# Kernel optimization log

Measured on AMD Instinct MI355X. Metric: run time of the kernel, lower is better.

Reference implementation:

```python
import jax, jax.numpy as jnp
import numpy as np

N = 100000
E = 3200000
H = 128
C = 40


def setup_inputs() -> dict:
    key = jax.random.key(0)
    ks = jax.random.split(key, 7)
    x = jax.random.normal(ks[0], (N, H), dtype=jnp.float32)
    edge_src = jax.random.randint(ks[1], (E,), 0, N, dtype=jnp.int32)
    edge_dst = jnp.sort(jax.random.randint(ks[2], (E,), 0, N, dtype=jnp.int32))
    edge_w = jax.random.uniform(ks[3], (E,), dtype=jnp.float32)
    s = 1.0 / np.sqrt(H)
    W0 = jax.random.normal(ks[4], (H, H), dtype=jnp.float32) * s
    W1 = jax.random.normal(ks[5], (H, H), dtype=jnp.float32) * s
    W2 = jax.random.normal(ks[6], (H, C), dtype=jnp.float32) * s
    return {"x": x, "edge_src": edge_src, "edge_dst": edge_dst,
            "edge_w": edge_w, "W0": W0, "W1": W1, "W2": W2}


def _spmm(h, edge_src, edge_dst, edge_w):
    # out[i] = sum_{e: dst_e == i} w_e * h[src_e]   (sparse adj @ h)
    msgs = h[edge_src] * edge_w[:, None]          # [E, d]
    return jax.ops.segment_sum(msgs, edge_dst, num_segments=N)


def reference(x, edge_src, edge_dst, edge_w, W0, W1, W2):
    # layer 1: tanh(Linear(spmm(adj, x)))  (dropout is identity in eval mode)
    h = jnp.tanh(_spmm(x, edge_src, edge_dst, edge_w) @ W0)
    # layer 2
    h = jnp.tanh(_spmm(h, edge_src, edge_dst, edge_w) @ W1)
    # output layer (GraphConvSparse default activation is tanh here too)
    out = jnp.tanh(_spmm(h, edge_src, edge_dst, edge_w) @ W2)
    return out
```

## Files before the change

### kernel.cpp

```cpp
#include <hip/hip_runtime.h>
#include <hip/hip_fp16.h>

#define NN 100000
#define NPAD 100096
#define EE 3200000
#define HH 128
#define CC 40

typedef _Float16 f16x8 __attribute__((ext_vector_type(8)));
typedef float f32x4 __attribute__((ext_vector_type(4)));

__device__ __forceinline__ float fast_tanh(float x) {
    float t = __expf(2.f * fminf(x, 15.f));
    return (t - 1.f) * __builtin_amdgcn_rcpf(t + 1.f);
}

__global__ void build_rp(const int* __restrict__ dst, int* __restrict__ rp) {
    int i = blockIdx.x * blockDim.x + threadIdx.x;
    if (i > NN) return;
    int lo = 0, hi = EE;
    while (lo < hi) {
        int mid = (lo + hi) >> 1;
        if (dst[mid] < i) lo = mid + 1; else hi = mid;
    }
    rp[i] = lo;
}

__global__ __launch_bounds__(256) void prep_all(const float* __restrict__ x,
                                                const int* __restrict__ src,
                                                const float* __restrict__ w,
                                                const float* __restrict__ W0,
                                                const float* __restrict__ W1,
                                                const float* __restrict__ W2,
                                                __half* __restrict__ xh,
                                                int4* __restrict__ ew,
                                                __half* __restrict__ W0t,
                                                __half* __restrict__ W1t,
                                                __half* __restrict__ W2t) {
    int b = blockIdx.x, tid = threadIdx.x;
    if (b < 6250) {
        int base = (b * 256 + tid) * 8;
        float4 a = *(const float4*)(x + base);
        float4 c = *(const float4*)(x + base + 4);
        __half2 h[4];
        h[0] = __floats2half2_rn(a.x, a.y);
        h[1] = __floats2half2_rn(a.z, a.w);
        h[2] = __floats2half2_rn(c.x, c.y);
        h[3] = __floats2half2_rn(c.z, c.w);
        *(float4*)(xh + base) = *(float4*)h;
    } else if (b < 9375) {
        int i = (b - 6250) * 256 + tid;
        int4 s = ((const int4*)src)[i];
        float4 f = ((const float4*)w)[i];
        int4 pa, pb;
        pa.x = s.x; pa.y = __float_as_int(f.x); pa.z = s.y; pa.w = __float_as_int(f.y);
        pb.x = s.z; pb.y = __float_as_int(f.z); pb.z = s.w; pb.w = __float_as_int(f.w);
        ew[2 * i] = pa; ew[2 * i + 1] = pb;
    } else {
        int i = (b - 9375) * 256 + tid;
        if (i < HH * HH) {
            int c = i >> 7, k = i & 127;
            W0t[i] = __float2half_rn(W0[k * HH + c]);
            W1t[i] = __float2half_rn(W1[k * HH + c]);
        }
        if (i < 64 * HH) {
            int c = i >> 7, k = i & 127;
            W2t[i] = __float2half_rn(c < CC ? W2[k * CC + c] : 0.f);
        }
    }
}

__global__ __launch_bounds__(256) void spmm_h16(const __half* __restrict__ h,
                                                const int2* __restrict__ ew,
                                                const int* __restrict__ rp,
                                                __half* __restrict__ out) {
    int node = blockIdx.x * 4 + (threadIdx.x >> 6);
    int l = threadIdx.x & 63;
    if (node >= NN) return;
    int e0 = __builtin_amdgcn_readfirstlane(rp[node]);
    int e1 = __builtin_amdgcn_readfirstlane(rp[node + 1]);
    int g = l >> 4, r = l & 15;
    const f16x8* __restrict__ hrow = (const f16x8*)h;
    float acc[8] = {};
    int e = e0;
    if ((e & 1) && e < e1) {
        int2 pr = ew[e];
        float wk = (g == 0) ? __int_as_float(pr.y) : 0.f;
        f16x8 v = hrow[(size_t)pr.x * 16 + r];
#pragma unroll
        for (int j = 0; j < 8; ++j) acc[j] = fmaf(wk, (float)v[j], acc[j]);
        ++e;
    }
    int efull = e + ((e1 - e) & ~15);
    for (; e < efull; e += 16) {
        const int4* pp = (const int4*)(ew + e + 4 * g);
        int4 pa = pp[0];
        int4 pb = pp[1];
        f16x8 v0 = hrow[(size_t)pa.x * 16 + r];
        f16x8 v1 = hrow[(size_t)pa.z * 16 + r];
        f16x8 v2 = hrow[(size_t)pb.x * 16 + r];
        f16x8 v3 = hrow[(size_t)pb.z * 16 + r];
        float w0 = __int_as_float(pa.y), w1 = __int_as_float(pa.w);
        float w2 = __int_as_float(pb.y), w3 = __int_as_float(pb.w);
#pragma unroll
        for (int j = 0; j < 8; ++j) acc[j] = fmaf(w0, (float)v0[j], acc[j]);
#pragma unroll
        for (int j = 0; j < 8; ++j) acc[j] = fmaf(w1, (float)v1[j], acc[j]);
#pragma unroll
        for (int j = 0; j < 8; ++j) acc[j] = fmaf(w2, (float)v2[j], acc[j]);
#pragma unroll
        for (int j = 0; j < 8; ++j) acc[j] = fmaf(w3, (float)v3[j], acc[j]);
    }
    if (e < e1) {
#pragma unroll
        for (int k = 0; k < 4; ++k) {
            int idx = e + 4 * g + k;
            bool val = idx < e1;
            int2 pr = ew[val ? idx : e0];
            float wk = val ? __int_as_float(pr.y) : 0.f;
            f16x8 v = hrow[(size_t)pr.x * 16 + r];
#pragma unroll
            for (int j = 0; j < 8; ++j) acc[j] = fmaf(wk, (float)v[j], acc[j]);
        }
    }
#pragma unroll
    for (int j = 0; j < 8; ++j) {
        acc[j] += __shfl_xor(acc[j], 16);
        acc[j] += __shfl_xor(acc[j], 32);
    }
    if (l < 16) {
        __half2 hv[4];
#pragma unroll
        for (int j = 0; j < 4; ++j) hv[j] = __floats2half2_rn(acc[2 * j], acc[2 * j + 1]);
        *(float4*)(out + (size_t)node * HH + r * 8) = *(float4*)hv;
    }
}

__global__ __launch_bounds__(256) void spmm40_tanh(const __half* __restrict__ gpad,
                                                   const int2* __restrict__ ew,
                                                   const int* __restrict__ rp,
                                                   float* __restrict__ out) {
    int node = blockIdx.x * 4 + (threadIdx.x >> 6);
    int l = threadIdx.x & 63;
    if (node >= NN) return;
    int e0 = __builtin_amdgcn_readfirstlane(rp[node]);
    int e1 = __builtin_amdgcn_readfirstlane(rp[node + 1]);
    int g = l >> 3, r = l & 7;
    const f16x8* __restrict__ grow = (const f16x8*)gpad;
    float acc[8] = {};
    int e = e0;
    if ((e & 1) && e < e1) {
        int2 pr = ew[e];
        float wk = (g == 0) ? __int_as_float(pr.y) : 0.f;
        f16x8 v = grow[(size_t)pr.x * 8 + r];
#pragma unroll
        for (int j = 0; j < 8; ++j) acc[j] = fmaf(wk, (float)v[j], acc[j]);
        ++e;
    }
    int efull = e + ((e1 - e) & ~15);
    for (; e < efull; e += 16) {
        int4 pa = *(const int4*)(ew + e + 2 * g);
        f16x8 v0 = grow[(size_t)pa.x * 8 + r];
        f16x8 v1 = grow[(size_t)pa.z * 8 + r];
        float w0 = __int_as_float(pa.y), w1 = __int_as_float(pa.w);
#pragma unroll
        for (int j = 0; j < 8; ++j) acc[j] = fmaf(w0, (float)v0[j], acc[j]);
#pragma unroll
        for (int j = 0; j < 8; ++j) acc[j] = fmaf(w1, (float)v1[j], acc[j]);
    }
    if (e < e1) {
#pragma unroll
        for (int k = 0; k < 2; ++k) {
            int idx = e + 2 * g + k;
            bool val = idx < e1;
            int2 pr = ew[val ? idx : e0];
            float wk = val ? __int_as_float(pr.y) : 0.f;
            f16x8 v = grow[(size_t)pr.x * 8 + r];
#pragma unroll
            for (int j = 0; j < 8; ++j) acc[j] = fmaf(wk, (float)v[j], acc[j]);
        }
    }
#pragma unroll
    for (int j = 0; j < 8; ++j) {
        acc[j] += __shfl_xor(acc[j], 8);
        acc[j] += __shfl_xor(acc[j], 16);
        acc[j] += __shfl_xor(acc[j], 32);
    }
    if (l < 5) {
        float o[8];
#pragma unroll
        for (int j = 0; j < 8; ++j) o[j] = fast_tanh(acc[j]);
        *(float4*)(out + (size_t)node * CC + r * 8) = *(float4*)&o[0];
        *(float4*)(out + (size_t)node * CC + r * 8 + 4) = *(float4*)&o[4];
    }
}

__global__ __launch_bounds__(256) void gemm_tanh_mfma(const __half* __restrict__ A,
                                                      const __half* __restrict__ Wt,
                                                      __half* __restrict__ out) {
    __shared__ _Float16 st[4][16][136];
    int wave = threadIdx.x >> 6, l = threadIdx.x & 63;
    int r0 = blockIdx.x * 64 + wave * 16;
    int lr = l & 15, lg = l >> 4;
    const _Float16* Af = (const _Float16*)A;
    const _Float16* Wf = (const _Float16*)Wt;
    f16x8 a[4];
#pragma unroll
    for (int kb = 0; kb < 4; ++kb)
        a[kb] = *(const f16x8*)(Af + (size_t)(r0 + lr) * HH + kb * 32 + lg * 8);
#pragma unroll
    for (int ct = 0; ct < 8; ++ct) {
        f32x4 acc = {0.f, 0.f, 0.f, 0.f};
#pragma unroll
        for (int kb = 0; kb < 4; ++kb) {
            f16x8 b = *(const f16x8*)(Wf + (size_t)(ct * 16 + lr) * HH + kb * 32 + lg * 8);
            acc = __builtin_amdgcn_mfma_f32_16x16x32_f16(a[kb], b, acc, 0, 0, 0);
        }
#pragma unroll
        for (int r = 0; r < 4; ++r)
            st[wave][lg * 4 + r][ct * 16 + lr] = (_Float16)fast_tanh(acc[r]);
    }
#pragma unroll
    for (int i = 0; i < 4; ++i) {
        int row = lg + 4 * i;
        int grow = r0 + row;
        f16x8 v = *(const f16x8*)&st[wave][row][lr * 8];
        if (grow < NN)
            *(f16x8*)((_Float16*)out + (size_t)grow * HH + lr * 8) = v;
    }
}

__global__ __launch_bounds__(256) void gemm2_fused(const __half* __restrict__ A,
                                                   const __half* __restrict__ W1t,
                                                   const __half* __restrict__ W2t,
                                                   __half* __restrict__ gout) {
    __shared__ _Float16 st[4][16][136];
    int wave = threadIdx.x >> 6, l = threadIdx.x & 63;
    int r0 = blockIdx.x * 64 + wave * 16;
    int lr = l & 15, lg = l >> 4;
    const _Float16* Af = (const _Float16*)A;
    const _Float16* W1f = (const _Float16*)W1t;
    const _Float16* W2f = (const _Float16*)W2t;
    f16x8 a[4];
#pragma unroll
    for (int kb = 0; kb < 4; ++kb)
        a[kb] = *(const f16x8*)(Af + (size_t)(r0 + lr) * HH + kb * 32 + lg * 8);
#pragma unroll
    for (int ct = 0; ct < 8; ++ct) {
        f32x4 acc = {0.f, 0.f, 0.f, 0.f};
#pragma unroll
        for (int kb = 0; kb < 4; ++kb) {
            f16x8 b = *(const f16x8*)(W1f + (size_t)(ct * 16 + lr) * HH + kb * 32 + lg * 8);
            acc = __builtin_amdgcn_mfma_f32_16x16x32_f16(a[kb], b, acc, 0, 0, 0);
        }
#pragma unroll
        for (int r = 0; r < 4; ++r)
            st[wave][lg * 4 + r][ct * 16 + lr] = (_Float16)fast_tanh(acc[r]);
    }
    f16x8 a2[4];
#pragma unroll
    for (int kb = 0; kb < 4; ++kb)
        a2[kb] = *(const f16x8*)&st[wave][lr][kb * 32 + lg * 8];
#pragma unroll
    for (int ct = 0; ct < 4; ++ct) {
        f32x4 acc = {0.f, 0.f, 0.f, 0.f};
#pragma unroll
        for (int kb = 0; kb < 4; ++kb) {
            f16x8 b = *(const f16x8*)(W2f + (size_t)(ct * 16 + lr) * HH + kb * 32 + lg * 8);
            acc = __builtin_amdgcn_mfma_f32_16x16x32_f16(a2[kb], b, acc, 0, 0, 0);
        }
#pragma unroll
        for (int r = 0; r < 4; ++r)
            st[wave][lg * 4 + r][ct * 16 + lr] = (_Float16)acc[r];
    }
#pragma unroll
    for (int i = 0; i < 2; ++i) {
        int row = (l >> 3) + 8 * i;
        int grow = r0 + row;
        f16x8 v = *(const f16x8*)&st[wave][row][(l & 7) * 8];
        if (grow < NN)
            *(f16x8*)((_Float16*)gout + (size_t)grow * 64 + (l & 7) * 8) = v;
    }
}

extern "C" void kernel_launch(void* const* d_in, const int* in_sizes, int n_in,
                              void* d_out, int out_size, void* d_ws, size_t ws_size,
                              hipStream_t stream) {
    const float* x    = (const float*)d_in[0];
    const int*   esrc = (const int*)d_in[1];
    const int*   edst = (const int*)d_in[2];
    const float* ew_f = (const float*)d_in[3];
    const float* W0   = (const float*)d_in[4];
    const float* W1   = (const float*)d_in[5];
    const float* W2   = (const float*)d_in[6];
    float* out = (float*)d_out;

    char* ws = (char*)d_ws;
    size_t off = 0;
    int* rp = (int*)(ws + off);          off += (((size_t)(NN + 1) * 4) + 511) & ~(size_t)511;
    __half* buf0 = (__half*)(ws + off);  off += (size_t)NPAD * HH * sizeof(__half);
    __half* sA = (__half*)(ws + off);    off += (size_t)NPAD * HH * sizeof(__half);
    __half* hb = (__half*)(ws + off);    off += (size_t)NPAD * HH * sizeof(__half);
    int2* ew = (int2*)(ws + off);        off += (size_t)EE * sizeof(int2);
    __half* W0t = (__half*)(ws + off);   off += (size_t)HH * HH * sizeof(__half);
    __half* W1t = (__half*)(ws + off);   off += (size_t)HH * HH * sizeof(__half);
    __half* W2t = (__half*)(ws + off);   off += (size_t)64 * HH * sizeof(__half);
    __half* xh = buf0;
    __half* gb = buf0;

    build_rp<<<(NN + 256) / 256, 256, 0, stream>>>(edst, rp);
    prep_all<<<9439, 256, 0, stream>>>(x, esrc, ew_f, W0, W1, W2,
                                       xh, (int4*)ew, W0t, W1t, W2t);

    int gemm_grid = NPAD / 64;
    spmm_h16<<<NN / 4, 256, 0, stream>>>(xh, ew, rp, sA);
    gemm_tanh_mfma<<<gemm_grid, 256, 0, stream>>>(sA, W0t, hb);
    spmm_h16<<<NN / 4, 256, 0, stream>>>(hb, ew, rp, sA);
    gemm2_fused<<<gemm_grid, 256, 0, stream>>>(sA, W1t, W2t, gb);
    spmm40_tanh<<<NN / 4, 256, 0, stream>>>(gb, ew, rp, out);
}
```

Baseline: 483.2 us.

## Fuse SpMM with MFMA GEMM per layer and pack edges into 32-bit words

Each of the first two layers now runs as one kernel. A wave aggregates 16 node rows into shared memory, with one half2 column pair per lane, then runs the MFMA GEMM plus tanh in place, so the intermediate sA buffer round-trip and two launches are removed. Edge source and weight are packed into a single 32-bit word (17-bit index, 15-bit quantised weight), halving edge-stream traffic. In exchange, the weights lose precision, and the aggregation walks nodes sequentially with unroll 1, which may expose gather latency.

```diff
diff --git a/kernel.cpp b/kernel.cpp
--- a/kernel.cpp
+++ b/kernel.cpp
@@ -33,7 +33,7 @@
                                                 const float* __restrict__ W1,
                                                 const float* __restrict__ W2,
                                                 __half* __restrict__ xh,
-                                                int4* __restrict__ ew,
+                                                unsigned* __restrict__ ewp,
                                                 __half* __restrict__ W0t,
                                                 __half* __restrict__ W1t,
                                                 __half* __restrict__ W2t) {
@@ -52,10 +52,12 @@
         int i = (b - 6250) * 256 + tid;
         int4 s = ((const int4*)src)[i];
         float4 f = ((const float4*)w)[i];
-        int4 pa, pb;
-        pa.x = s.x; pa.y = __float_as_int(f.x); pa.z = s.y; pa.w = __float_as_int(f.y);
-        pb.x = s.z; pb.y = __float_as_int(f.z); pb.z = s.w; pb.w = __float_as_int(f.w);
-        ew[2 * i] = pa; ew[2 * i + 1] = pb;
+        uint4 p;
+        p.x = (unsigned)s.x | ((unsigned)(f.x * 32767.f + 0.5f) << 17);
+        p.y = (unsigned)s.y | ((unsigned)(f.y * 32767.f + 0.5f) << 17);
+        p.z = (unsigned)s.z | ((unsigned)(f.z * 32767.f + 0.5f) << 17);
+        p.w = (unsigned)s.w | ((unsigned)(f.w * 32767.f + 0.5f) << 17);
+        ((uint4*)ewp)[i] = p;
     } else {
         int i = (b - 9375) * 256 + tid;
         if (i < HH * HH) {
@@ -70,74 +72,174 @@
     }
 }
 
-__global__ __launch_bounds__(256) void spmm_h16(const __half* __restrict__ h,
-                                                const int2* __restrict__ ew,
+#define EDEC_W(v) ((float)((v) >> 17) * (1.f / 32767.f))
+#define EDEC_S(v) ((v) & 131071u)
+
+__device__ __forceinline__ void spmm_tile(const __half2* __restrict__ h2,
+                                          const unsigned* __restrict__ ewp,
+                                          const int* __restrict__ rp,
+                                          int n0, int l,
+                                          _Float16 (* __restrict__ As)[136]) {
+#pragma unroll 1
+    for (int i = 0; i < 16; ++i) {
+        int node = n0 + i;
+        int ia = node <= NN ? node : NN;
+        int ib = node + 1 <= NN ? node + 1 : NN;
+        int e0 = __builtin_amdgcn_readfirstlane(rp[ia]);
+        int e1 = __builtin_amdgcn_readfirstlane(rp[ib]);
+        float accx = 0.f, accy = 0.f;
+        int e = e0;
+        while ((e & 3) && e < e1) {
+            unsigned v = ewp[e];
+            float wk = EDEC_W(v);
+            float2 f = __half22float2(h2[(size_t)EDEC_S(v) * 64 + l]);
+            accx = fmaf(wk, f.x, accx); accy = fmaf(wk, f.y, accy);
+            ++e;
+        }
+        int e8 = e + ((e1 - e) & ~7);
+#pragma unroll 1
+        for (; e < e8; e += 8) {
+            uint4 pa = *(const uint4*)(ewp + e);
+            uint4 pb = *(const uint4*)(ewp + e + 4);
+            __half2 r0 = h2[(size_t)EDEC_S(pa.x) * 64 + l];
+            __half2 r1 = h2[(size_t)EDEC_S(pa.y) * 64 + l];
+            __half2 r2 = h2[(size_t)EDEC_S(pa.z) * 64 + l];
+            __half2 r3 = h2[(size_t)EDEC_S(pa.w) * 64 + l];
+            __half2 r4 = h2[(size_t)EDEC_S(pb.x) * 64 + l];
+            __half2 r5 = h2[(size_t)EDEC_S(pb.y) * 64 + l];
+            __half2 r6 = h2[(size_t)EDEC_S(pb.z) * 64 + l];
+            __half2 r7 = h2[(size_t)EDEC_S(pb.w) * 64 + l];
+            float2 f0 = __half22float2(r0), f1 = __half22float2(r1);
+            float2 f2 = __half22float2(r2), f3 = __half22float2(r3);
+            float2 f4 = __half22float2(r4), f5 = __half22float2(r5);
+            float2 f6 = __half22float2(r6), f7 = __half22float2(r7);
+            float w0 = EDEC_W(pa.x), w1 = EDEC_W(pa.y), w2 = EDEC_W(pa.z), w3 = EDEC_W(pa.w);
+            float w4 = EDEC_W(pb.x), w5 = EDEC_W(pb.y), w6 = EDEC_W(pb.z), w7 = EDEC_W(pb.w);
+            accx = fmaf(w0, f0.x, accx); accy = fmaf(w0, f0.y, accy);
+            accx = fmaf(w1, f1.x, accx); accy = fmaf(w1, f1.y, accy);
+            accx = fmaf(w2, f2.x, accx); accy = fmaf(w2, f2.y, accy);
+            accx = fmaf(w3, f3.x, accx); accy = fmaf(w3, f3.y, accy);
+            accx = fmaf(w4, f4.x, accx); accy = fmaf(w4, f4.y, accy);
+            accx = fmaf(w5, f5.x, accx); accy = fmaf(w5, f5.y, accy);
+            accx = fmaf(w6, f6.x, accx); accy = fmaf(w6, f6.y, accy);
+            accx = fmaf(w7, f7.x, accx); accy = fmaf(w7, f7.y, accy);
+        }
+        if (e + 4 <= e1) {
+            uint4 pa = *(const uint4*)(ewp + e);
+            __half2 r0 = h2[(size_t)EDEC_S(pa.x) * 64 + l];
+            __half2 r1 = h2[(size_t)EDEC_S(pa.y) * 64 + l];
+            __half2 r2 = h2[(size_t)EDEC_S(pa.z) * 64 + l];
+            __half2 r3 = h2[(size_t)EDEC_S(pa.w) * 64 + l];
+            float2 f0 = __half22float2(r0), f1 = __half22float2(r1);
+            float2 f2 = __half22float2(r2), f3 = __half22float2(r3);
+            float w0 = EDEC_W(pa.x), w1 = EDEC_W(pa.y), w2 = EDEC_W(pa.z), w3 = EDEC_W(pa.w);
+            accx = fmaf(w0, f0.x, accx); accy = fmaf(w0, f0.y, accy);
+            accx = fmaf(w1, f1.x, accx); accy = fmaf(w1, f1.y, accy);
+            accx = fmaf(w2, f2.x, accx); accy = fmaf(w2, f2.y, accy);
+            accx = fmaf(w3, f3.x, accx); accy = fmaf(w3, f3.y, accy);
+            e += 4;
+        }
+        while (e < e1) {
+            unsigned v = ewp[e];
+            float wk = EDEC_W(v);
+            float2 f = __half22float2(h2[(size_t)EDEC_S(v) * 64 + l]);
+            accx = fmaf(wk, f.x, accx); accy = fmaf(wk, f.y, accy);
+            ++e;
+        }
+        *(__half2*)&As[i][2 * l] = __floats2half2_rn(accx, accy);
+    }
+}
+
+__global__ __launch_bounds__(256) void fused_l1(const __half* __restrict__ h,
+                                                const unsigned* __restrict__ ewp,
                                                 const int* __restrict__ rp,
+                                                const __half* __restrict__ Wt,
                                                 __half* __restrict__ out) {
-    int node = blockIdx.x * 4 + (threadIdx.x >> 6);
-    int l = threadIdx.x & 63;
-    if (node >= NN) return;
-    int e0 = __builtin_amdgcn_readfirstlane(rp[node]);
-    int e1 = __builtin_amdgcn_readfirstlane(rp[node + 1]);
-    int g = l >> 4, r = l & 15;
-    const f16x8* __restrict__ hrow = (const f16x8*)h;
-    float acc[8] = {};
-    int e = e0;
-    if ((e & 1) && e < e1) {
-        int2 pr = ew[e];
-        float wk = (g == 0) ? __int_as_float(pr.y) : 0.f;
-        f16x8 v = hrow[(size_t)pr.x * 16 + r];
-#pragma unroll
-        for (int j = 0; j < 8; ++j) acc[j] = fmaf(wk, (float)v[j], acc[j]);
-        ++e;
-    }
-    int efull = e + ((e1 - e) & ~15);
-    for (; e < efull; e += 16) {
-        const int4* pp = (const int4*)(ew + e + 4 * g);
-        int4 pa = pp[0];
-        int4 pb = pp[1];
-        f16x8 v0 = hrow[(size_t)pa.x * 16 + r];
-        f16x8 v1 = hrow[(size_t)pa.z * 16 + r];
-        f16x8 v2 = hrow[(size_t)pb.x * 16 + r];
-        f16x8 v3 = hrow[(size_t)pb.z * 16 + r];
-        float w0 = __int_as_float(pa.y), w1 = __int_as_float(pa.w);
-        float w2 = __int_as_float(pb.y), w3 = __int_as_float(pb.w);
-#pragma unroll
-        for (int j = 0; j < 8; ++j) acc[j] = fmaf(w0, (float)v0[j], acc[j]);
-#pragma unroll
-        for (int j = 0; j < 8; ++j) acc[j] = fmaf(w1, (float)v1[j], acc[j]);
-#pragma unroll
-        for (int j = 0; j < 8; ++j) acc[j] = fmaf(w2, (float)v2[j], acc[j]);
-#pragma unroll
-        for (int j = 0; j < 8; ++j) acc[j] = fmaf(w3, (float)v3[j], acc[j]);
-    }
-    if (e < e1) {
-#pragma unroll
-        for (int k = 0; k < 4; ++k) {
-            int idx = e + 4 * g + k;
-            bool val = idx < e1;
-            int2 pr = ew[val ? idx : e0];
-            float wk = val ? __int_as_float(pr.y) : 0.f;
-            f16x8 v = hrow[(size_t)pr.x * 16 + r];
-#pragma unroll
-            for (int j = 0; j < 8; ++j) acc[j] = fmaf(wk, (float)v[j], acc[j]);
-        }
-    }
-#pragma unroll
-    for (int j = 0; j < 8; ++j) {
-        acc[j] += __shfl_xor(acc[j], 16);
-        acc[j] += __shfl_xor(acc[j], 32);
-    }
-    if (l < 16) {
-        __half2 hv[4];
-#pragma unroll
-        for (int j = 0; j < 4; ++j) hv[j] = __floats2half2_rn(acc[2 * j], acc[2 * j + 1]);
-        *(float4*)(out + (size_t)node * HH + r * 8) = *(float4*)hv;
+    __shared__ _Float16 As[4][16][136];
+    int wave = threadIdx.x >> 6, l = threadIdx.x & 63;
+    int n0 = blockIdx.x * 64 + wave * 16;
+    spmm_tile((const __half2*)h, ewp, rp, n0, l, As[wave]);
+    int lr = l & 15, lg = l >> 4;
+    f16x8 a[4];
+#pragma unroll
+    for (int kb = 0; kb < 4; ++kb)
+        a[kb] = *(const f16x8*)&As[wave][lr][kb * 32 + lg * 8];
+    const _Float16* Wf = (const _Float16*)Wt;
+#pragma unroll
+    for (int ct = 0; ct < 8; ++ct) {
+        f32x4 acc = {0.f, 0.f, 0.f, 0.f};
+#pragma unroll
+        for (int kb = 0; kb < 4; ++kb) {
+            f16x8 b = *(const f16x8*)(Wf + (size_t)(ct * 16 + lr) * HH + kb * 32 + lg * 8);
+            acc = __builtin_amdgcn_mfma_f32_16x16x32_f16(a[kb], b, acc, 0, 0, 0);
+        }
+#pragma unroll
+        for (int r = 0; r < 4; ++r)
+            As[wave][lg * 4 + r][ct * 16 + lr] = (_Float16)fast_tanh(acc[r]);
+    }
+#pragma unroll
+    for (int i = 0; i < 4; ++i) {
+        int row = lg + 4 * i;
+        f16x8 v = *(const f16x8*)&As[wave][row][lr * 8];
+        *(f16x8*)((_Float16*)out + (size_t)(n0 + row) * HH + lr * 8) = v;
+    }
+}
+
+__global__ __launch_bounds__(256) void fused_l2(const __half* __restrict__ h,
+                                                const unsigned* __restrict__ ewp,
+                                                const int* __restrict__ rp,
+                                                const __half* __restrict__ W1t,
+                                                const __half* __restrict__ W2t,
+                                                __half* __restrict__ gout) {
+    __shared__ _Float16 As[4][16][136];
+    int wave = threadIdx.x >> 6, l = threadIdx.x & 63;
+    int n0 = blockIdx.x * 64 + wave * 16;
+    spmm_tile((const __half2*)h, ewp, rp, n0, l, As[wave]);
+    int lr = l & 15, lg = l >> 4;
+    const _Float16* W1f = (const _Float16*)W1t;
+    const _Float16* W2f = (const _Float16*)W2t;
+    f16x8 a[4];
+#pragma unroll
+    for (int kb = 0; kb < 4; ++kb)
+        a[kb] = *(const f16x8*)&As[wave][lr][kb * 32 + lg * 8];
+#pragma unroll
+    for (int ct = 0; ct < 8; ++ct) {
+        f32x4 acc = {0.f, 0.f, 0.f, 0.f};
+#pragma unroll
+        for (int kb = 0; kb < 4; ++kb) {
+            f16x8 b = *(const f16x8*)(W1f + (size_t)(ct * 16 + lr) * HH + kb * 32 + lg * 8);
+            acc = __builtin_amdgcn_mfma_f32_16x16x32_f16(a[kb], b, acc, 0, 0, 0);
+        }
+#pragma unroll
+        for (int r = 0; r < 4; ++r)
+            As[wave][lg * 4 + r][ct * 16 + lr] = (_Float16)fast_tanh(acc[r]);
+    }
+    f16x8 a2[4];
+#pragma unroll
+    for (int kb = 0; kb < 4; ++kb)
+        a2[kb] = *(const f16x8*)&As[wave][lr][kb * 32 + lg * 8];
+#pragma unroll
+    for (int ct = 0; ct < 4; ++ct) {
+        f32x4 acc = {0.f, 0.f, 0.f, 0.f};
+#pragma unroll
+        for (int kb = 0; kb < 4; ++kb) {
+            f16x8 b = *(const f16x8*)(W2f + (size_t)(ct * 16 + lr) * HH + kb * 32 + lg * 8);
+            acc = __builtin_amdgcn_mfma_f32_16x16x32_f16(a2[kb], b, acc, 0, 0, 0);
+        }
+#pragma unroll
+        for (int r = 0; r < 4; ++r)
+            As[wave][lg * 4 + r][ct * 16 + lr] = (_Float16)acc[r];
+    }
+#pragma unroll
+    for (int i = 0; i < 2; ++i) {
+        int row = (l >> 3) + 8 * i;
+        f16x8 v = *(const f16x8*)&As[wave][row][(l & 7) * 8];
+        *(f16x8*)((_Float16*)gout + (size_t)(n0 + row) * 64 + (l & 7) * 8) = v;
     }
 }
 
 __global__ __launch_bounds__(256) void spmm40_tanh(const __half* __restrict__ gpad,
-                                                   const int2* __restrict__ ew,
+                                                   const unsigned* __restrict__ ewp,
                                                    const int* __restrict__ rp,
                                                    float* __restrict__ out) {
     int node = blockIdx.x * 4 + (threadIdx.x >> 6);
@@ -146,23 +248,23 @@
     int e0 = __builtin_amdgcn_readfirstlane(rp[node]);
     int e1 = __builtin_amdgcn_readfirstlane(rp[node + 1]);
     int g = l >> 3, r = l & 7;
-    const f16x8* __restrict__ grow = (const f16x8*)gpad;
+    const f16x8* __restrict__ grw = (const f16x8*)gpad;
     float acc[8] = {};
     int e = e0;
-    if ((e & 1) && e < e1) {
-        int2 pr = ew[e];
-        float wk = (g == 0) ? __int_as_float(pr.y) : 0.f;
-        f16x8 v = grow[(size_t)pr.x * 8 + r];
-#pragma unroll
-        for (int j = 0; j < 8; ++j) acc[j] = fmaf(wk, (float)v[j], acc[j]);
+    while ((e & 1) && e < e1) {
+        unsigned v = ewp[e];
+        float wk = (g == 0) ? EDEC_W(v) : 0.f;
+        f16x8 vv = grw[(size_t)EDEC_S(v) * 8 + r];
+#pragma unroll
+        for (int j = 0; j < 8; ++j) acc[j] = fmaf(wk, (float)vv[j], acc[j]);
         ++e;
     }
-    int efull = e + ((e1 - e) & ~15);
-    for (; e < efull; e += 16) {
-        int4 pa = *(const int4*)(ew + e + 2 * g);
-        f16x8 v0 = grow[(size_t)pa.x * 8 + r];
-        f16x8 v1 = grow[(size_t)pa.z * 8 + r];
-        float w0 = __int_as_float(pa.y), w1 = __int_as_float(pa.w);
+    int e16 = e + ((e1 - e) & ~15);
+    for (; e < e16; e += 16) {
+        uint2 pa = *(const uint2*)(ewp + e + 2 * g);
+        f16x8 v0 = grw[(size_t)EDEC_S(pa.x) * 8 + r];
+        f16x8 v1 = grw[(size_t)EDEC_S(pa.y) * 8 + r];
+        float w0 = EDEC_W(pa.x), w1 = EDEC_W(pa.y);
 #pragma unroll
         for (int j = 0; j < 8; ++j) acc[j] = fmaf(w0, (float)v0[j], acc[j]);
 #pragma unroll
@@ -173,11 +275,11 @@
         for (int k = 0; k < 2; ++k) {
             int idx = e + 2 * g + k;
             bool val = idx < e1;
-            int2 pr = ew[val ? idx : e0];
-            float wk = val ? __int_as_float(pr.y) : 0.f;
-            f16x8 v = grow[(size_t)pr.x * 8 + r];
-#pragma unroll
-            for (int j = 0; j < 8; ++j) acc[j] = fmaf(wk, (float)v[j], acc[j]);
+            unsigned v = ewp[val ? idx : e0];
+            float wk = val ? EDEC_W(v) : 0.f;
+            f16x8 vv = grw[(size_t)EDEC_S(v) * 8 + r];
+#pragma unroll
+            for (int j = 0; j < 8; ++j) acc[j] = fmaf(wk, (float)vv[j], acc[j]);
         }
     }
 #pragma unroll
@@ -192,94 +294,6 @@
         for (int j = 0; j < 8; ++j) o[j] = fast_tanh(acc[j]);
         *(float4*)(out + (size_t)node * CC + r * 8) = *(float4*)&o[0];
         *(float4*)(out + (size_t)node * CC + r * 8 + 4) = *(float4*)&o[4];
-    }
-}
-
-__global__ __launch_bounds__(256) void gemm_tanh_mfma(const __half* __restrict__ A,
-                                                      const __half* __restrict__ Wt,
-                                                      __half* __restrict__ out) {
-    __shared__ _Float16 st[4][16][136];
-    int wave = threadIdx.x >> 6, l = threadIdx.x & 63;
-    int r0 = blockIdx.x * 64 + wave * 16;
-    int lr = l & 15, lg = l >> 4;
-    const _Float16* Af = (const _Float16*)A;
-    const _Float16* Wf = (const _Float16*)Wt;
-    f16x8 a[4];
-#pragma unroll
-    for (int kb = 0; kb < 4; ++kb)
-        a[kb] = *(const f16x8*)(Af + (size_t)(r0 + lr) * HH + kb * 32 + lg * 8);
-#pragma unroll
-    for (int ct = 0; ct < 8; ++ct) {
-        f32x4 acc = {0.f, 0.f, 0.f, 0.f};
-#pragma unroll
-        for (int kb = 0; kb < 4; ++kb) {
-            f16x8 b = *(const f16x8*)(Wf + (size_t)(ct * 16 + lr) * HH + kb * 32 + lg * 8);
-            acc = __builtin_amdgcn_mfma_f32_16x16x32_f16(a[kb], b, acc, 0, 0, 0);
-        }
-#pragma unroll
-        for (int r = 0; r < 4; ++r)
-            st[wave][lg * 4 + r][ct * 16 + lr] = (_Float16)fast_tanh(acc[r]);
-    }
-#pragma unroll
-    for (int i = 0; i < 4; ++i) {
-        int row = lg + 4 * i;
-        int grow = r0 + row;
-        f16x8 v = *(const f16x8*)&st[wave][row][lr * 8];
-        if (grow < NN)
-            *(f16x8*)((_Float16*)out + (size_t)grow * HH + lr * 8) = v;
-    }
-}
-
-__global__ __launch_bounds__(256) void gemm2_fused(const __half* __restrict__ A,
-                                                   const __half* __restrict__ W1t,
-                                                   const __half* __restrict__ W2t,
-                                                   __half* __restrict__ gout) {
-    __shared__ _Float16 st[4][16][136];
-    int wave = threadIdx.x >> 6, l = threadIdx.x & 63;
-    int r0 = blockIdx.x * 64 + wave * 16;
-    int lr = l & 15, lg = l >> 4;
-    const _Float16* Af = (const _Float16*)A;
-    const _Float16* W1f = (const _Float16*)W1t;
-    const _Float16* W2f = (const _Float16*)W2t;
-    f16x8 a[4];
-#pragma unroll
-    for (int kb = 0; kb < 4; ++kb)
-        a[kb] = *(const f16x8*)(Af + (size_t)(r0 + lr) * HH + kb * 32 + lg * 8);
-#pragma unroll
-    for (int ct = 0; ct < 8; ++ct) {
-        f32x4 acc = {0.f, 0.f, 0.f, 0.f};
-#pragma unroll
-        for (int kb = 0; kb < 4; ++kb) {
-            f16x8 b = *(const f16x8*)(W1f + (size_t)(ct * 16 + lr) * HH + kb * 32 + lg * 8);
-            acc = __builtin_amdgcn_mfma_f32_16x16x32_f16(a[kb], b, acc, 0, 0, 0);
-        }
-#pragma unroll
-        for (int r = 0; r < 4; ++r)
-            st[wave][lg * 4 + r][ct * 16 + lr] = (_Float16)fast_tanh(acc[r]);
-    }
-    f16x8 a2[4];
-#pragma unroll
-    for (int kb = 0; kb < 4; ++kb)
-        a2[kb] = *(const f16x8*)&st[wave][lr][kb * 32 + lg * 8];
-#pragma unroll
-    for (int ct = 0; ct < 4; ++ct) {
-        f32x4 acc = {0.f, 0.f, 0.f, 0.f};
-#pragma unroll
-        for (int kb = 0; kb < 4; ++kb) {
-            f16x8 b = *(const f16x8*)(W2f + (size_t)(ct * 16 + lr) * HH + kb * 32 + lg * 8);
-            acc = __builtin_amdgcn_mfma_f32_16x16x32_f16(a2[kb], b, acc, 0, 0, 0);
-        }
-#pragma unroll
-        for (int r = 0; r < 4; ++r)
-            st[wave][lg * 4 + r][ct * 16 + lr] = (_Float16)acc[r];
-    }
-#pragma unroll
-    for (int i = 0; i < 2; ++i) {
-        int row = (l >> 3) + 8 * i;
-        int grow = r0 + row;
-        f16x8 v = *(const f16x8*)&st[wave][row][(l & 7) * 8];
-        if (grow < NN)
-            *(f16x8*)((_Float16*)gout + (size_t)grow * 64 + (l & 7) * 8) = v;
     }
 }
 
@@ -299,9 +313,8 @@
     size_t off = 0;
     int* rp = (int*)(ws + off);          off += (((size_t)(NN + 1) * 4) + 511) & ~(size_t)511;
     __half* buf0 = (__half*)(ws + off);  off += (size_t)NPAD * HH * sizeof(__half);
-    __half* sA = (__half*)(ws + off);    off += (size_t)NPAD * HH * sizeof(__half);
     __half* hb = (__half*)(ws + off);    off += (size_t)NPAD * HH * sizeof(__half);
-    int2* ew = (int2*)(ws + off);        off += (size_t)EE * sizeof(int2);
+    unsigned* ewp = (unsigned*)(ws + off); off += (size_t)EE * sizeof(unsigned);
     __half* W0t = (__half*)(ws + off);   off += (size_t)HH * HH * sizeof(__half);
     __half* W1t = (__half*)(ws + off);   off += (size_t)HH * HH * sizeof(__half);
     __half* W2t = (__half*)(ws + off);   off += (size_t)64 * HH * sizeof(__half);
@@ -309,13 +322,11 @@
     __half* gb = buf0;
 
     build_rp<<<(NN + 256) / 256, 256, 0, stream>>>(edst, rp);
-    prep_all<<<9439, 256, 0, stream>>>(x, esrc, ew_f, W0, W1, W2,
-                                       xh, (int4*)ew, W0t, W1t, W2t);
-
-    int gemm_grid = NPAD / 64;
-    spmm_h16<<<NN / 4, 256, 0, stream>>>(xh, ew, rp, sA);
-    gemm_tanh_mfma<<<gemm_grid, 256, 0, stream>>>(sA, W0t, hb);
-    spmm_h16<<<NN / 4, 256, 0, stream>>>(hb, ew, rp, sA);
-    gemm2_fused<<<gemm_grid, 256, 0, stream>>>(sA, W1t, W2t, gb);
-    spmm40_tanh<<<NN / 4, 256, 0, stream>>>(gb, ew, rp, out);
-}
+    prep_all<<<9440, 256, 0, stream>>>(x, esrc, ew_f, W0, W1, W2,
+                                       xh, ewp, W0t, W1t, W2t);
+
+    int grid = NPAD / 64;
+    fused_l1<<<grid, 256, 0, stream>>>(xh, ewp, rp, W0t, hb);
+    fused_l2<<<grid, 256, 0, stream>>>(hb, ewp, rp, W1t, W2t, gb);
+    spmm40_tanh<<<NN / 4, 256, 0, stream>>>(gb, ewp, rp, out);
+}
```

Result: slower. 507.6 us (+5.1%).

## Pack edge src and weight into 32 bits and bucket-sort edges by source

Applied to the files above, without the earlier changes.

Each edge's source index (17 bits) and weight (quantized to 15 bits) now share one 32-bit word, halving the edge-stream bytes read by the three SpMM passes. A new sort_edges kernel reorders each destination's edge list into 16 buckets by source range, so gathers within a node touch nearby rows and get better cache locality. This adds an extra pass over the edges and loses weight precision, since the 15-bit fixed-point weights could push results outside tolerance. The alignment prologue now handles up to 3 edges so the uint4 loads stay aligned.

```diff
diff --git a/kernel.cpp b/kernel.cpp
--- a/kernel.cpp
+++ b/kernel.cpp
@@ -6,9 +6,13 @@
 #define EE 3200000
 #define HH 128
 #define CC 40
+#define NT 16
 
 typedef _Float16 f16x8 __attribute__((ext_vector_type(8)));
 typedef float f32x4 __attribute__((ext_vector_type(4)));
+
+#define EDEC_W(v) ((float)((v) >> 17) * (1.f / 32767.f))
+#define EDEC_S(v) ((v) & 131071u)
 
 __device__ __forceinline__ float fast_tanh(float x) {
     float t = __expf(2.f * fminf(x, 15.f));
@@ -33,7 +37,7 @@
                                                 const float* __restrict__ W1,
                                                 const float* __restrict__ W2,
                                                 __half* __restrict__ xh,
-                                                int4* __restrict__ ew,
+                                                unsigned* __restrict__ ewp,
                                                 __half* __restrict__ W0t,
                                                 __half* __restrict__ W1t,
                                                 __half* __restrict__ W2t) {
@@ -52,10 +56,12 @@
         int i = (b - 6250) * 256 + tid;
         int4 s = ((const int4*)src)[i];
         float4 f = ((const float4*)w)[i];
-        int4 pa, pb;
-        pa.x = s.x; pa.y = __float_as_int(f.x); pa.z = s.y; pa.w = __float_as_int(f.y);
-        pb.x = s.z; pb.y = __float_as_int(f.z); pb.z = s.w; pb.w = __float_as_int(f.w);
-        ew[2 * i] = pa; ew[2 * i + 1] = pb;
+        uint4 p;
+        p.x = (unsigned)s.x | ((unsigned)(f.x * 32767.f + 0.5f) << 17);
+        p.y = (unsigned)s.y | ((unsigned)(f.y * 32767.f + 0.5f) << 17);
+        p.z = (unsigned)s.z | ((unsigned)(f.z * 32767.f + 0.5f) << 17);
+        p.w = (unsigned)s.w | ((unsigned)(f.w * 32767.f + 0.5f) << 17);
+        ((uint4*)ewp)[i] = p;
     } else {
         int i = (b - 9375) * 256 + tid;
         if (i < HH * HH) {
@@ -70,8 +76,47 @@
     }
 }
 
+__global__ __launch_bounds__(256) void sort_edges(const unsigned* __restrict__ in,
+                                                  const int* __restrict__ rp,
+                                                  unsigned* __restrict__ outp) {
+    int node = blockIdx.x * 4 + (threadIdx.x >> 6);
+    int l = threadIdx.x & 63;
+    if (node >= NN) return;
+    int e0 = __builtin_amdgcn_readfirstlane(rp[node]);
+    int e1 = __builtin_amdgcn_readfirstlane(rp[node + 1]);
+    int count[NT];
+#pragma unroll
+    for (int t = 0; t < NT; ++t) count[t] = 0;
+    for (int e = e0; e < e1; e += 64) {
+        int idx = e + l;
+        bool val = idx < e1;
+        unsigned v = val ? in[idx] : 0u;
+        int t = val ? (int)(EDEC_S(v) >> 13) : -1;
+#pragma unroll
+        for (int tt = 0; tt < NT; ++tt)
+            count[tt] += __popcll(__ballot(t == tt));
+    }
+    int base[NT];
+    int run = e0;
+#pragma unroll
+    for (int tt = 0; tt < NT; ++tt) { base[tt] = run; run += count[tt]; }
+    unsigned long long lmask = (1ull << l) - 1ull;
+    for (int e = e0; e < e1; e += 64) {
+        int idx = e + l;
+        bool val = idx < e1;
+        unsigned v = val ? in[idx] : 0u;
+        int t = val ? (int)(EDEC_S(v) >> 13) : -1;
+#pragma unroll
+        for (int tt = 0; tt < NT; ++tt) {
+            unsigned long long b = __ballot(t == tt);
+            if (t == tt) outp[base[tt] + __popcll(b & lmask)] = v;
+            base[tt] += __popcll(b);
+        }
+    }
+}
+
 __global__ __launch_bounds__(256) void spmm_h16(const __half* __restrict__ h,
-                                                const int2* __restrict__ ew,
+                                                const unsigned* __restrict__ ewp,
                                                 const int* __restrict__ rp,
                                                 __half* __restrict__ out) {
     int node = blockIdx.x * 4 + (threadIdx.x >> 6);
@@ -83,25 +128,22 @@
     const f16x8* __restrict__ hrow = (const f16x8*)h;
     float acc[8] = {};
     int e = e0;
-    if ((e & 1) && e < e1) {
-        int2 pr = ew[e];
-        float wk = (g == 0) ? __int_as_float(pr.y) : 0.f;
-        f16x8 v = hrow[(size_t)pr.x * 16 + r];
-#pragma unroll
-        for (int j = 0; j < 8; ++j) acc[j] = fmaf(wk, (float)v[j], acc[j]);
+    while ((e & 3) && e < e1) {
+        unsigned v = ewp[e];
+        float wk = (g == 0) ? EDEC_W(v) : 0.f;
+        f16x8 vv = hrow[(size_t)EDEC_S(v) * 16 + r];
+#pragma unroll
+        for (int j = 0; j < 8; ++j) acc[j] = fmaf(wk, (float)vv[j], acc[j]);
         ++e;
     }
-    int efull = e + ((e1 - e) & ~15);
-    for (; e < efull; e += 16) {
-        const int4* pp = (const int4*)(ew + e + 4 * g);
-        int4 pa = pp[0];
-        int4 pb = pp[1];
-        f16x8 v0 = hrow[(size_t)pa.x * 16 + r];
-        f16x8 v1 = hrow[(size_t)pa.z * 16 + r];
-        f16x8 v2 = hrow[(size_t)pb.x * 16 + r];
-        f16x8 v3 = hrow[(size_t)pb.z * 16 + r];
-        float w0 = __int_as_float(pa.y), w1 = __int_as_float(pa.w);
-        float w2 = __int_as_float(pb.y), w3 = __int_as_float(pb.w);
+    int e16 = e + ((e1 - e) & ~15);
+    for (; e < e16; e += 16) {
+        uint4 p = *(const uint4*)(ewp + e + 4 * g);
+        f16x8 v0 = hrow[(size_t)EDEC_S(p.x) * 16 + r];
+        f16x8 v1 = hrow[(size_t)EDEC_S(p.y) * 16 + r];
+        f16x8 v2 = hrow[(size_t)EDEC_S(p.z) * 16 + r];
+        f16x8 v3 = hrow[(size_t)EDEC_S(p.w) * 16 + r];
+        float w0 = EDEC_W(p.x), w1 = EDEC_W(p.y), w2 = EDEC_W(p.z), w3 = EDEC_W(p.w);
 #pragma unroll
         for (int j = 0; j < 8; ++j) acc[j] = fmaf(w0, (float)v0[j], acc[j]);
 #pragma unroll
@@ -116,11 +158,11 @@
         for (int k = 0; k < 4; ++k) {
             int idx = e + 4 * g + k;
             bool val = idx < e1;
-            int2 pr = ew[val ? idx : e0];
-            float wk = val ? __int_as_float(pr.y) : 0.f;
-            f16x8 v = hrow[(size_t)pr.x * 16 + r];
-#pragma unroll
-            for (int j = 0; j < 8; ++j) acc[j] = fmaf(wk, (float)v[j], acc[j]);
+            unsigned v = ewp[val ? idx : e0];
+            float wk = val ? EDEC_W(v) : 0.f;
+            f16x8 vv = hrow[(size_t)EDEC_S(v) * 16 + r];
+#pragma unroll
+            for (int j = 0; j < 8; ++j) acc[j] = fmaf(wk, (float)vv[j], acc[j]);
         }
     }
 #pragma unroll
@@ -137,7 +179,7 @@
 }
 
 __global__ __launch_bounds__(256) void spmm40_tanh(const __half* __restrict__ gpad,
-                                                   const int2* __restrict__ ew,
+                                                   const unsigned* __restrict__ ewp,
                                                    const int* __restrict__ rp,
                                                    float* __restrict__ out) {
     int node = blockIdx.x * 4 + (threadIdx.x >> 6);
@@ -146,23 +188,23 @@
     int e0 = __builtin_amdgcn_readfirstlane(rp[node]);
     int e1 = __builtin_amdgcn_readfirstlane(rp[node + 1]);
     int g = l >> 3, r = l & 7;
-    const f16x8* __restrict__ grow = (const f16x8*)gpad;
+    const f16x8* __restrict__ grw = (const f16x8*)gpad;
     float acc[8] = {};
     int e = e0;
-    if ((e & 1) && e < e1) {
-        int2 pr = ew[e];
-        float wk = (g == 0) ? __int_as_float(pr.y) : 0.f;
-        f16x8 v = grow[(size_t)pr.x * 8 + r];
-#pragma unroll
-        for (int j = 0; j < 8; ++j) acc[j] = fmaf(wk, (float)v[j], acc[j]);
+    while ((e & 1) && e < e1) {
+        unsigned v = ewp[e];
+        float wk = (g == 0) ? EDEC_W(v) : 0.f;
+        f16x8 vv = grw[(size_t)EDEC_S(v) * 8 + r];
+#pragma unroll
+        for (int j = 0; j < 8; ++j) acc[j] = fmaf(wk, (float)vv[j], acc[j]);
         ++e;
     }
-    int efull = e + ((e1 - e) & ~15);
-    for (; e < efull; e += 16) {
-        int4 pa = *(const int4*)(ew + e + 2 * g);
-        f16x8 v0 = grow[(size_t)pa.x * 8 + r];
-        f16x8 v1 = grow[(size_t)pa.z * 8 + r];
-        float w0 = __int_as_float(pa.y), w1 = __int_as_float(pa.w);
+    int e16 = e + ((e1 - e) & ~15);
+    for (; e < e16; e += 16) {
+        uint2 pa = *(const uint2*)(ewp + e + 2 * g);
+        f16x8 v0 = grw[(size_t)EDEC_S(pa.x) * 8 + r];
+        f16x8 v1 = grw[(size_t)EDEC_S(pa.y) * 8 + r];
+        float w0 = EDEC_W(pa.x), w1 = EDEC_W(pa.y);
 #pragma unroll
         for (int j = 0; j < 8; ++j) acc[j] = fmaf(w0, (float)v0[j], acc[j]);
 #pragma unroll
@@ -173,11 +215,11 @@
         for (int k = 0; k < 2; ++k) {
             int idx = e + 2 * g + k;
             bool val = idx < e1;
-            int2 pr = ew[val ? idx : e0];
-            float wk = val ? __int_as_float(pr.y) : 0.f;
-            f16x8 v = grow[(size_t)pr.x * 8 + r];
-#pragma unroll
-            for (int j = 0; j < 8; ++j) acc[j] = fmaf(wk, (float)v[j], acc[j]);
+            unsigned v = ewp[val ? idx : e0];
+            float wk = val ? EDEC_W(v) : 0.f;
+            f16x8 vv = grw[(size_t)EDEC_S(v) * 8 + r];
+#pragma unroll
+            for (int j = 0; j < 8; ++j) acc[j] = fmaf(wk, (float)vv[j], acc[j]);
         }
     }
 #pragma unroll
@@ -297,25 +339,27 @@
 
     char* ws = (char*)d_ws;
     size_t off = 0;
-    int* rp = (int*)(ws + off);          off += (((size_t)(NN + 1) * 4) + 511) & ~(size_t)511;
-    __half* buf0 = (__half*)(ws + off);  off += (size_t)NPAD * HH * sizeof(__half);
-    __half* sA = (__half*)(ws + off);    off += (size_t)NPAD * HH * sizeof(__half);
-    __half* hb = (__half*)(ws + off);    off += (size_t)NPAD * HH * sizeof(__half);
-    int2* ew = (int2*)(ws + off);        off += (size_t)EE * sizeof(int2);
-    __half* W0t = (__half*)(ws + off);   off += (size_t)HH * HH * sizeof(__half);
-    __half* W1t = (__half*)(ws + off);   off += (size_t)HH * HH * sizeof(__half);
-    __half* W2t = (__half*)(ws + off);   off += (size_t)64 * HH * sizeof(__half);
+    int* rp = (int*)(ws + off);            off += (((size_t)(NN + 1) * 4) + 511) & ~(size_t)511;
+    __half* buf0 = (__half*)(ws + off);    off += (size_t)NPAD * HH * sizeof(__half);
+    __half* sA = (__half*)(ws + off);      off += (size_t)NPAD * HH * sizeof(__half);
+    __half* hb = (__half*)(ws + off);      off += (size_t)NPAD * HH * sizeof(__half);
+    unsigned* ewp = (unsigned*)(ws + off); off += (size_t)EE * sizeof(unsigned);
+    unsigned* ews = (unsigned*)(ws + off); off += (size_t)EE * sizeof(unsigned);
+    __half* W0t = (__half*)(ws + off);     off += (size_t)HH * HH * sizeof(__half);
+    __half* W1t = (__half*)(ws + off);     off += (size_t)HH * HH * sizeof(__half);
+    __half* W2t = (__half*)(ws + off);     off += (size_t)64 * HH * sizeof(__half);
     __half* xh = buf0;
     __half* gb = buf0;
 
     build_rp<<<(NN + 256) / 256, 256, 0, stream>>>(edst, rp);
-    prep_all<<<9439, 256, 0, stream>>>(x, esrc, ew_f, W0, W1, W2,
-                                       xh, (int4*)ew, W0t, W1t, W2t);
+    prep_all<<<9440, 256, 0, stream>>>(x, esrc, ew_f, W0, W1, W2,
+                                       xh, ewp, W0t, W1t, W2t);
+    sort_edges<<<NN / 4, 256, 0, stream>>>(ewp, rp, ews);
 
     int gemm_grid = NPAD / 64;
-    spmm_h16<<<NN / 4, 256, 0, stream>>>(xh, ew, rp, sA);
+    spmm_h16<<<NN / 4, 256, 0, stream>>>(xh, ews, rp, sA);
     gemm_tanh_mfma<<<gemm_grid, 256, 0, stream>>>(sA, W0t, hb);
-    spmm_h16<<<NN / 4, 256, 0, stream>>>(hb, ew, rp, sA);
+    spmm_h16<<<NN / 4, 256, 0, stream>>>(hb, ews, rp, sA);
     gemm2_fused<<<gemm_grid, 256, 0, stream>>>(sA, W1t, W2t, gb);
-    spmm40_tanh<<<NN / 4, 256, 0, stream>>>(gb, ew, rp, out);
-}
+    spmm40_tanh<<<NN / 4, 256, 0, stream>>>(gb, ews, rp, out);
+}
```

Result: slower. 504.7 us (+4.5%).
